# Kernel tuning notes

Hardware: AMD Instinct MI355X
Metric: run time of the kernel (lower is better)

## Reference

```python
import jax, jax.numpy as jnp
import numpy as np

N = 50000      # nodes
E = 300000     # edges per hop
H = 64         # hidden_channels
P = 3          # hops
DIRS = 3
L = 2          # num_layers
G = 50         # graphs in batch
FUS_IN = H * (2 + 2 * DIRS)  # 512
SLOPE = 0.01   # torch leaky_relu default negative slope


def setup_inputs():
    key = jax.random.key(0)
    ks = jax.random.split(key, 32)
    def nrm(k, shape, s=0.1):
        return jax.random.normal(k, shape, jnp.float32) * s
    return {
        "x": jax.random.normal(ks[0], (N, H), jnp.float32),
        "pe": jax.random.normal(ks[1], (N, DIRS), jnp.float32),
        "batch": jnp.sort(jax.random.randint(ks[2], (N,), 0, G, jnp.int32)),
        "u_edge_index": jax.random.randint(ks[3], (P, 2, E), 0, N, jnp.int32),
        "u_edge_weight": jax.random.uniform(ks[4], (P, E), jnp.float32),
        "f_edge_index": jax.random.randint(ks[5], (P, 2, E), 0, N, jnp.int32),
        "f_edge_weight": jax.random.uniform(ks[6], (P, E), jnp.float32),
        "emb_W": nrm(ks[7], (H, H)), "emb_b": nrm(ks[8], (H,)),
        "S_lin_W": nrm(ks[9], (L, H, H)), "S_lin_b": nrm(ks[10], (L, H)),
        "S_d": nrm(ks[11], (L, P, H), 1.0), "S_hb": nrm(ks[12], (L, P, H)),
        "S_fW": nrm(ks[13], (L, P, FUS_IN, H), 0.04), "S_fb": nrm(ks[14], (L, P, H)),
        "F_lin_W": nrm(ks[15], (L, H, H)), "F_lin_b": nrm(ks[16], (L, H)),
        "F_d": nrm(ks[17], (L, P, H), 1.0), "F_hb": nrm(ks[18], (L, P, H)),
        "F_fW": nrm(ks[19], (L, P, FUS_IN, H), 0.04), "F_fb": nrm(ks[20], (L, P, H)),
        "nS_w": 1.0 + nrm(ks[21], (L, H)), "nS_b": nrm(ks[22], (L, H)),
        "nS_m": 1.0 + nrm(ks[23], (L, H)),
        "nF_w": 1.0 + nrm(ks[24], (L, H)), "nF_b": nrm(ks[25], (L, H)),
        "nF_m": 1.0 + nrm(ks[26], (L, H)),
        "gate_W": nrm(ks[27], (2 * H, H)), "gate_b": nrm(ks[28], (H,)),
    }


def _opdmp(x, pe, ei, ew, lin_W, lin_b, d, hop_bias, fus_W, fus_b):
    """One OPDMPConv: multi-hop gather / scatter_add with directional weights."""
    x_t = x @ lin_W + lin_b              # [N, H]
    d_w = jax.nn.softmax(d, axis=0)      # [P, H]
    out = jnp.zeros_like(x_t)
    u = pe[:, :DIRS]
    for p in range(P):
        row, col, w = ei[p, 0], ei[p, 1], ew[p]
        # precompute() runs under torch.no_grad() -> stop_gradient
        deg = jax.ops.segment_sum(jax.lax.stop_gradient(w), row, num_segments=N)
        deg_inv = jnp.where(deg == 0.0, 0.0, 1.0 / deg)                  # [N]
        diff = jax.lax.stop_gradient(u[col] - u[row])                    # [E, DIRS]
        W2 = jnp.concatenate([jax.nn.relu(diff), jax.nn.relu(-diff)], axis=1)  # [E, 2*DIRS]
        xc = x_t[col]                                                    # [E, H] gather
        out_avg = jax.ops.segment_sum(xc * w[:, None], row, num_segments=N) * deg_inv[:, None]
        msg_dir = (xc[:, :, None] * W2[:, None, :]).reshape(E, H * 2 * DIRS)
        out_dir = jax.ops.segment_sum(msg_dir, row, num_segments=N) * deg_inv[:, None]
        h_cat = jnp.concatenate([x_t, out_avg, out_dir], axis=-1)        # [N, FUS_IN]
        h_p = jax.nn.leaky_relu(h_cat @ fus_W[p] + fus_b[p], SLOPE)
        out = out + h_p * d_w[p] + hop_bias[p]
    return out


def _graph_norm(x, batch, w, b, ms):
    cnt = jnp.maximum(jax.ops.segment_sum(jnp.ones((N,), x.dtype), batch, num_segments=G), 1.0)
    mean = jax.ops.segment_sum(x, batch, num_segments=G) / cnt[:, None]
    out = x - mean[batch] * ms
    var = jax.ops.segment_sum(out * out, batch, num_segments=G) / cnt[:, None]
    return out / jnp.sqrt(var[batch] + 1e-5) * w + b


def _forward(x, pe, u_edge_weight, f_edge_weight, emb_W, emb_b,
             S_lin_W, S_lin_b, S_d, S_hb, S_fW, S_fb,
             F_lin_W, F_lin_b, F_d, F_hb, F_fW, F_fb,
             nS_w, nS_b, nS_m, nF_w, nF_b, nF_m,
             gate_W, gate_b, batch, u_edge_index, f_edge_index):
    x = x @ emb_W + emb_b
    for i in range(L):
        prev = x
        h = _opdmp(x, pe, u_edge_index, u_edge_weight,
                   S_lin_W[i], S_lin_b[i], S_d[i], S_hb[i], S_fW[i], S_fb[i])
        h = jax.nn.leaky_relu(_graph_norm(h, batch, nS_w[i], nS_b[i], nS_m[i]), SLOPE)
        fx = _opdmp(h, pe, f_edge_index, f_edge_weight,
                    F_lin_W[i], F_lin_b[i], F_d[i], F_hb[i], F_fW[i], F_fb[i])
        fx = jax.nn.leaky_relu(_graph_norm(fx, batch, nF_w[i], nF_b[i], nF_m[i]), SLOPE)
        gate = jax.nn.sigmoid(jnp.concatenate([h, fx], axis=-1) @ gate_W + gate_b)
        x = gate * h + (1.0 - gate) * fx + prev   # dropout = identity in eval mode
    cnt = jnp.maximum(jax.ops.segment_sum(jnp.ones((N,), x.dtype), batch, num_segments=G), 1.0)
    return jax.ops.segment_sum(x, batch, num_segments=G) / cnt[:, None]  # global_mean_pool


def reference(x, pe, batch, u_edge_index, u_edge_weight, f_edge_index, f_edge_weight,
              emb_W, emb_b, S_lin_W, S_lin_b, S_d, S_hb, S_fW, S_fb,
              F_lin_W, F_lin_b, F_d, F_hb, F_fW, F_fb,
              nS_w, nS_b, nS_m, nF_w, nF_b, nF_m, gate_W, gate_b):
    return _forward(x, pe, u_edge_weight, f_edge_weight, emb_W, emb_b,
                    S_lin_W, S_lin_b, S_d, S_hb, S_fW, S_fb,
                    F_lin_W, F_lin_b, F_d, F_hb, F_fW, F_fb,
                    nS_w, nS_b, nS_m, nF_w, nF_b, nF_m,
                    gate_W, gate_b, batch, u_edge_index, f_edge_index)
```

## Files before the change

### kernel.cpp

```cpp
#include <hip/hip_runtime.h>
#include <cstdint>
#include <cstddef>

#define NN 50000
#define EE 300000
#define HH 64
#define PP 3
#define GG 50
#define LL 2
#define CAP 32
#define SLOPE 0.01f

typedef __attribute__((ext_vector_type(8))) short bf16x8;
typedef __attribute__((ext_vector_type(4))) float f32x4;

__device__ __forceinline__ float lrelu(float x){ return x >= 0.f ? x : SLOPE*x; }

__device__ __forceinline__ unsigned short f2bf(float x){
    uint32_t u = __float_as_uint(x);
    uint32_t r = (u + 0x7FFFu + ((u >> 16) & 1u)) >> 16;
    return (unsigned short)r;
}

__global__ void k_bounds(const int* __restrict__ batch, int* __restrict__ gstart){
    int g = threadIdx.x;
    if (g > GG) return;
    int lo = 0, hi = NN;
    while (lo < hi){ int mid = (lo + hi) >> 1; if (batch[mid] < g) lo = mid + 1; else hi = mid; }
    gstart[g] = lo;
}

__global__ void k_pe4(const float* __restrict__ pe, float4* __restrict__ pe4){
    int n = blockIdx.x * blockDim.x + threadIdx.x;
    if (n >= NN) return;
    pe4[n] = make_float4(pe[n * 3 + 0], pe[n * 3 + 1], pe[n * 3 + 2], 0.f);
}

__global__ void k_fill2(const int* __restrict__ uei, const float* __restrict__ uew,
                        const int* __restrict__ fei, const float* __restrict__ few,
                        int* __restrict__ cnt, int2* __restrict__ bucket){
    int t = blockIdx.x * blockDim.x + threadIdx.x;
    if (t >= 2 * PP * EE) return;
    int which = t / EE;
    int e = t - which * EE;
    const int* ei; const float* ew; int p;
    if (which < PP){ ei = uei; ew = uew; p = which; }
    else           { ei = fei; ew = few; p = which - PP; }
    int row = ei[(size_t)(p * 2 + 0) * EE + e];
    int col = ei[(size_t)(p * 2 + 1) * EE + e];
    float w = ew[(size_t)p * EE + e];
    int slot = atomicAdd(cnt + (size_t)which * NN + row, 1);
    if (slot < CAP)
        bucket[((size_t)which * NN + row) * CAP + slot] = make_int2(col, __float_as_int(w));
}

__global__ void k_wpermb(const float* __restrict__ S_fW, const float* __restrict__ F_fW,
                         unsigned short* __restrict__ Wpb){
    int gid = blockIdx.x * blockDim.x + threadIdx.x;
    int j = gid & 7;
    int lane = (gid >> 3) & 63;
    int w = (gid >> 9) & 3;
    int kb = (gid >> 11) & 15;
    int t = gid >> 15;
    int q = kb * 32 + (lane >> 4) * 8 + j;
    int col = w * 16 + (lane & 15);
    int conv = t / 6, layer = (t % 6) / 3, p = t % 3;
    const float* src = (conv ? F_fW : S_fW) + ((size_t)layer * PP + p) * 512 * HH;
    int kref;
    if (q < 128) kref = q;
    else { int r = q - 128; kref = 128 + (r & 63) * 6 + (r >> 6); }
    Wpb[gid] = f2bf(src[(size_t)kref * HH + col]);
}

__global__ __launch_bounds__(256) void k_lin64(const float* __restrict__ X,
                       const float* __restrict__ W, const float* __restrict__ b,
                       float* __restrict__ out){
    __shared__ float xs[32][HH];
    int nb = blockIdx.x * 32;
    int t = threadIdx.x;
    #pragma unroll
    for (int i = 0; i < 2; ++i){
        int idx = t + 256 * i;
        int r = idx >> 4, c4 = idx & 15;
        int n = nb + r;
        float4 v = make_float4(0.f, 0.f, 0.f, 0.f);
        if (n < NN) v = *reinterpret_cast<const float4*>(X + (size_t)n * HH + c4 * 4);
        *reinterpret_cast<float4*>(&xs[r][c4 * 4]) = v;
    }
    __syncthreads();
    int lane = t & 63, wave = t >> 6, nw = wave * 8;
    float acc[8];
    float bb = b[lane];
    #pragma unroll
    for (int i = 0; i < 8; ++i) acc[i] = bb;
    #pragma unroll 2
    for (int k = 0; k < HH; ++k){
        float wv = W[(size_t)k * HH + lane];
        #pragma unroll
        for (int i = 0; i < 8; ++i) acc[i] += xs[nw + i][k] * wv;
    }
    #pragma unroll
    for (int i = 0; i < 8; ++i){
        int n = nb + nw + i;
        if (n < NN) out[(size_t)n * HH + lane] = acc[i];
    }
}

__global__ __launch_bounds__(256) void k_hop3(const float* __restrict__ xt,
        const int* __restrict__ cnt, const int2* __restrict__ bucket,
        const float4* __restrict__ pe4, const unsigned short* __restrict__ Wpb3,
        const float* __restrict__ fb3, const float* __restrict__ dmat,
        const float* __restrict__ hb3, float* __restrict__ outb){
    __shared__ unsigned short u[16][512];
    int nb = blockIdx.x * 16;
    int t = threadIdx.x;
    int lane = t & 63, wave = t >> 6, nw = wave * 4;
    {
        int r = t >> 4, c4 = t & 15;
        float4 v = *reinterpret_cast<const float4*>(xt + (size_t)(nb + r) * HH + c4 * 4);
        ushort4 s;
        s.x = f2bf(v.x); s.y = f2bf(v.y); s.z = f2bf(v.z); s.w = f2bf(v.w);
        int q = (c4 * 4) ^ ((r & 7) << 3);
        *reinterpret_cast<ushort4*>(&u[r][q]) = s;
    }
    int c = wave * 16 + (lane & 15);
    float d0 = dmat[c], d1 = dmat[64 + c], d2 = dmat[128 + c];
    float mx = fmaxf(d0, fmaxf(d1, d2));
    float e0 = expf(d0 - mx), e1 = expf(d1 - mx), e2 = expf(d2 - mx);
    float esum = e0 + e1 + e2;
    float dw0 = e0 / esum, dw1 = e1 / esum, dw2 = e2 / esum;
    float accOut[4];
    float hbs = hb3[c] + hb3[64 + c] + hb3[128 + c];
    #pragma unroll
    for (int r = 0; r < 4; ++r) accOut[r] = hbs;

    for (int p = 0; p < 3; ++p){
        __syncthreads();
        const int*  cntp = cnt + (size_t)p * NN;
        const int2* bp   = bucket + (size_t)p * NN * CAP;
        #pragma unroll
        for (int i = 0; i < 4; ++i){
            int n = nb + nw + i;
            float accA = 0.f, sumw = 0.f;
            float a0 = 0.f, a1 = 0.f, a2 = 0.f, a3 = 0.f, a4 = 0.f, a5 = 0.f;
            int len = cntp[n]; if (len > CAP) len = CAP;
            const int2* b = bp + (size_t)n * CAP;
            float4 pr = pe4[n];
            int  cols[8];
            float ws[8];
            #pragma unroll
            for (int s = 0; s < 8; ++s){
                int2 m = b[s];
                bool ok = (s < len);
                cols[s] = ok ? m.x : n;
                ws[s]   = ok ? __int_as_float(m.y) : 0.f;
            }
            float4 pcs[8];
            float  xvs[8];
            #pragma unroll
            for (int s = 0; s < 8; ++s){
                pcs[s] = pe4[cols[s]];
                xvs[s] = xt[(size_t)cols[s] * HH + lane];
            }
            #pragma unroll
            for (int s = 0; s < 8; ++s){
                float w = ws[s], xv = xvs[s];
                float dd0 = pcs[s].x - pr.x;
                float dd1 = pcs[s].y - pr.y;
                float dd2 = pcs[s].z - pr.z;
                sumw += w;  accA += w * xv;
                a0 += fmaxf(dd0, 0.f) * xv;  a3 += fmaxf(-dd0, 0.f) * xv;
                a1 += fmaxf(dd1, 0.f) * xv;  a4 += fmaxf(-dd1, 0.f) * xv;
                a2 += fmaxf(dd2, 0.f) * xv;  a5 += fmaxf(-dd2, 0.f) * xv;
            }
            for (int s = 8; s < len; ++s){
                int2 m = b[s];
                int col = m.x;
                float w = __int_as_float(m.y);
                float4 pc = pe4[col];
                float xv = xt[(size_t)col * HH + lane];
                float dd0 = pc.x - pr.x;
                float dd1 = pc.y - pr.y;
                float dd2 = pc.z - pr.z;
                sumw += w;  accA += w * xv;
                a0 += fmaxf(dd0, 0.f) * xv;  a3 += fmaxf(-dd0, 0.f) * xv;
                a1 += fmaxf(dd1, 0.f) * xv;  a4 += fmaxf(-dd1, 0.f) * xv;
                a2 += fmaxf(dd2, 0.f) * xv;  a5 += fmaxf(-dd2, 0.f) * xv;
            }
            float di = (sumw == 0.f) ? 0.f : 1.f / sumw;
            int il = nw + i;
            int sw = (il & 7) << 3;
            u[il][(64 + lane) ^ sw]           = f2bf(accA * di);
            u[il][(128 + 0 * 64 + lane) ^ sw] = f2bf(a0 * di);
            u[il][(128 + 1 * 64 + lane) ^ sw] = f2bf(a1 * di);
            u[il][(128 + 2 * 64 + lane) ^ sw] = f2bf(a2 * di);
            u[il][(128 + 3 * 64 + lane) ^ sw] = f2bf(a3 * di);
            u[il][(128 + 4 * 64 + lane) ^ sw] = f2bf(a4 * di);
            u[il][(128 + 5 * 64 + lane) ^ sw] = f2bf(a5 * di);
        }
        __syncthreads();
        const unsigned short* wb = Wpb3 + (size_t)p * 32768;
        f32x4 acc = {0.f, 0.f, 0.f, 0.f};
        int arow = lane & 15;
        int asw = (arow & 7) << 3;
        #pragma unroll
        for (int kb = 0; kb < 16; ++kb){
            int qa = (kb * 32 + (lane >> 4) * 8) ^ asw;
            bf16x8 a = *reinterpret_cast<const bf16x8*>(&u[arow][qa]);
            bf16x8 b = *reinterpret_cast<const bf16x8*>(&wb[(((size_t)kb * 4 + wave) * 64 + lane) * 8]);
            acc = __builtin_amdgcn_mfma_f32_16x16x32_bf16(a, b, acc, 0, 0, 0);
        }
        float fbv = fb3[p * 64 + c];
        float dw = (p == 0) ? dw0 : ((p == 1) ? dw1 : dw2);
        #pragma unroll
        for (int r = 0; r < 4; ++r)
            accOut[r] += lrelu(acc[r] + fbv) * dw;
    }
    #pragma unroll
    for (int r = 0; r < 4; ++r){
        int row = (lane >> 4) * 4 + r;
        outb[(size_t)(nb + row) * HH + c] = accOut[r];
    }
}

__global__ void k_stats(const float* __restrict__ X, const int* __restrict__ gstart,
                        float* __restrict__ sums, float* __restrict__ sumsq){
    int g = blockIdx.x;
    int tid = threadIdx.x;
    int o = tid & 63, sub = tid >> 6;
    int ns = gstart[g], ne = gstart[g + 1];
    float s = 0.f, q = 0.f;
    for (int n = ns + sub; n < ne; n += 16){
        float v = X[(size_t)n * 64 + o];
        s += v; q += v * v;
    }
    __shared__ float ls[16][64];
    __shared__ float lq[16][64];
    ls[sub][o] = s; lq[sub][o] = q;
    __syncthreads();
    if (sub == 0){
        #pragma unroll
        for (int k = 1; k < 16; ++k){ s += ls[k][o]; q += lq[k][o]; }
        sums[g * 64 + o] = s;
        sumsq[g * 64 + o] = q;
    }
}

__global__ void k_gnorm(float* __restrict__ X, const int* __restrict__ batch,
                        const int* __restrict__ gstart,
                        const float* __restrict__ sums, const float* __restrict__ sumsq,
                        const float* __restrict__ w, const float* __restrict__ b,
                        const float* __restrict__ ms){
    int gid = blockIdx.x * blockDim.x + threadIdx.x;
    if (gid >= NN * HH) return;
    int n = gid >> 6, o = gid & 63;
    int g = batch[n];
    float cnt = fmaxf((float)(gstart[g + 1] - gstart[g]), 1.f);
    float mean = sums[g * 64 + o] / cnt;
    float ex2 = sumsq[g * 64 + o] / cnt;
    float m = ms[o];
    float var = ex2 - mean * mean * m * (2.f - m);
    float v = (X[gid] - mean * m) * (1.f / sqrtf(var + 1e-5f)) * w[o] + b[o];
    X[gid] = lrelu(v);
}

__global__ __launch_bounds__(256) void k_gate2(const float* __restrict__ h,
                       const float* __restrict__ fx, const float* __restrict__ gW,
                       const float* __restrict__ gb, float* __restrict__ X){
    __shared__ float hs[32][HH];
    __shared__ float fs[32][HH];
    int nb = blockIdx.x * 32;
    int t = threadIdx.x;
    #pragma unroll
    for (int i = 0; i < 2; ++i){
        int idx = t + 256 * i;
        int r = idx >> 4, c4 = idx & 15;
        int n = nb + r;
        float4 vh = make_float4(0.f, 0.f, 0.f, 0.f);
        float4 vf = make_float4(0.f, 0.f, 0.f, 0.f);
        if (n < NN){
            vh = *reinterpret_cast<const float4*>(h  + (size_t)n * HH + c4 * 4);
            vf = *reinterpret_cast<const float4*>(fx + (size_t)n * HH + c4 * 4);
        }
        *reinterpret_cast<float4*>(&hs[r][c4 * 4]) = vh;
        *reinterpret_cast<float4*>(&fs[r][c4 * 4]) = vf;
    }
    __syncthreads();
    int lane = t & 63, wave = t >> 6, nw = wave * 8;
    float acc[8];
    float bb = gb[lane];
    #pragma unroll
    for (int i = 0; i < 8; ++i) acc[i] = bb;
    #pragma unroll 2
    for (int k = 0; k < HH; ++k){
        float w1 = gW[(size_t)k * HH + lane];
        float w2 = gW[(size_t)(64 + k) * HH + lane];
        #pragma unroll
        for (int i = 0; i < 8; ++i) acc[i] += hs[nw + i][k] * w1 + fs[nw + i][k] * w2;
    }
    #pragma unroll
    for (int i = 0; i < 8; ++i){
        int n = nb + nw + i;
        if (n < NN){
            float gt = 1.f / (1.f + expf(-acc[i]));
            float hv = hs[nw + i][lane];
            float fv = fs[nw + i][lane];
            size_t idx = (size_t)n * HH + lane;
            X[idx] = gt * hv + (1.f - gt) * fv + X[idx];
        }
    }
}

__global__ void k_finalout(const float* __restrict__ sums, const int* __restrict__ gstart,
                           float* __restrict__ out){
    int gid = blockIdx.x * blockDim.x + threadIdx.x;
    if (gid >= GG * HH) return;
    int g = gid >> 6;
    float cnt = fmaxf((float)(gstart[g + 1] - gstart[g]), 1.f);
    out[gid] = sums[gid] / cnt;
}

extern "C" void kernel_launch(void* const* d_in, const int* in_sizes, int n_in,
                              void* d_out, int out_size, void* d_ws, size_t ws_size,
                              hipStream_t stream) {
    const float* x_in   = (const float*)d_in[0];
    const float* pe     = (const float*)d_in[1];
    const int*   batch  = (const int*)d_in[2];
    const int*   uei    = (const int*)d_in[3];
    const float* uew    = (const float*)d_in[4];
    const int*   fei    = (const int*)d_in[5];
    const float* few    = (const float*)d_in[6];
    const float* emb_W  = (const float*)d_in[7];
    const float* emb_b  = (const float*)d_in[8];
    const float* S_lin_W= (const float*)d_in[9];
    const float* S_lin_b= (const float*)d_in[10];
    const float* S_d    = (const float*)d_in[11];
    const float* S_hb   = (const float*)d_in[12];
    const float* S_fW   = (const float*)d_in[13];
    const float* S_fb   = (const float*)d_in[14];
    const float* F_lin_W= (const float*)d_in[15];
    const float* F_lin_b= (const float*)d_in[16];
    const float* F_d    = (const float*)d_in[17];
    const float* F_hb   = (const float*)d_in[18];
    const float* F_fW   = (const float*)d_in[19];
    const float* F_fb   = (const float*)d_in[20];
    const float* nS_w   = (const float*)d_in[21];
    const float* nS_b   = (const float*)d_in[22];
    const float* nS_m   = (const float*)d_in[23];
    const float* nF_w   = (const float*)d_in[24];
    const float* nF_b   = (const float*)d_in[25];
    const float* nF_m   = (const float*)d_in[26];
    const float* gate_W = (const float*)d_in[27];
    const float* gate_b = (const float*)d_in[28];
    float* out = (float*)d_out;

    size_t off = 0;
    auto alloc = [&](size_t bytes)->void*{
        void* p = (char*)d_ws + off;
        off += (bytes + 255) & ~(size_t)255;
        return p;
    };
    float*  xbuf   = (float*)alloc((size_t)NN * HH * 4);
    float*  hbuf   = (float*)alloc((size_t)NN * HH * 4);
    float*  fxbuf  = (float*)alloc((size_t)NN * HH * 4);
    float*  xt     = (float*)alloc((size_t)NN * HH * 4);
    unsigned short* Wpb12 = (unsigned short*)alloc((size_t)12 * 32768 * 2);
    float4* pe4    = (float4*)alloc((size_t)NN * 16);
    int*    cnt    = (int*)  alloc((size_t)6 * NN * 4);
    int2*   bucket = (int2*) alloc((size_t)6 * NN * CAP * 8);
    int*    gstart = (int*)  alloc((GG + 1) * 4);
    float*  sums   = (float*)alloc(GG * HH * 4);
    float*  sumsq  = (float*)alloc(GG * HH * 4);

    const int BLK = 256;
    const int gridNH = (NN * HH) / BLK;
    const int gridN32 = (NN + 31) / 32;
    const int gridHop = NN / 16;
    const int gridEdges = (2 * PP * EE + BLK - 1) / BLK;
    const int gridWb = (12 * 32768) / BLK;

    k_bounds<<<1, 64, 0, stream>>>(batch, gstart);
    k_pe4<<<(NN + BLK - 1) / BLK, BLK, 0, stream>>>(pe, pe4);
    hipMemsetAsync(cnt, 0, (size_t)6 * NN * 4, stream);
    k_fill2<<<gridEdges, BLK, 0, stream>>>(uei, uew, fei, few, cnt, bucket);
    k_wpermb<<<gridWb, BLK, 0, stream>>>(S_fW, F_fW, Wpb12);
    k_lin64<<<gridN32, BLK, 0, stream>>>(x_in, emb_W, emb_b, xbuf);

    auto gnorm = [&](float* X, const float* w, const float* b, const float* ms){
        k_stats<<<GG, 1024, 0, stream>>>(X, gstart, sums, sumsq);
        k_gnorm<<<gridNH, BLK, 0, stream>>>(X, batch, gstart, sums, sumsq, w, b, ms);
    };

    for (int i = 0; i < LL; ++i){
        k_lin64<<<gridN32, BLK, 0, stream>>>(xbuf, S_lin_W + (size_t)i * HH * HH,
                                             S_lin_b + (size_t)i * HH, xt);
        k_hop3<<<gridHop, BLK, 0, stream>>>(xt, cnt, bucket, pe4,
                Wpb12 + (size_t)(0 * 6 + i * 3) * 32768,
                S_fb + (size_t)i * PP * HH, S_d + (size_t)i * PP * HH,
                S_hb + (size_t)i * PP * HH, hbuf);
        gnorm(hbuf, nS_w + (size_t)i * HH, nS_b + (size_t)i * HH, nS_m + (size_t)i * HH);
        k_lin64<<<gridN32, BLK, 0, stream>>>(hbuf, F_lin_W + (size_t)i * HH * HH,
                                             F_lin_b + (size_t)i * HH, xt);
        k_hop3<<<gridHop, BLK, 0, stream>>>(xt, cnt + (size_t)PP * NN,
                bucket + (size_t)PP * NN * CAP, pe4,
                Wpb12 + (size_t)(1 * 6 + i * 3) * 32768,
                F_fb + (size_t)i * PP * HH, F_d + (size_t)i * PP * HH,
                F_hb + (size_t)i * PP * HH, fxbuf);
        gnorm(fxbuf, nF_w + (size_t)i * HH, nF_b + (size_t)i * HH, nF_m + (size_t)i * HH);
        k_gate2<<<gridN32, BLK, 0, stream>>>(hbuf, fxbuf, gate_W, gate_b, xbuf);
    }

    k_stats<<<GG, 1024, 0, stream>>>(xbuf, gstart, sums, sumsq);
    k_finalout<<<(GG * HH + BLK - 1) / BLK, BLK, 0, stream>>>(sums, gstart, out);
}
```

Baseline: 1.220 ms.

## Store transformed features in bf16, batch second gather chunk, split graph stats

```diff
diff --git a/kernel.cpp b/kernel.cpp
--- a/kernel.cpp
+++ b/kernel.cpp
@@ -20,6 +20,9 @@
     uint32_t u = __float_as_uint(x);
     uint32_t r = (u + 0x7FFFu + ((u >> 16) & 1u)) >> 16;
     return (unsigned short)r;
+}
+__device__ __forceinline__ float bf2f(unsigned short s){
+    return __uint_as_float((uint32_t)s << 16);
 }
 
 __global__ void k_bounds(const int* __restrict__ batch, int* __restrict__ gstart){
@@ -106,7 +109,41 @@
     }
 }
 
-__global__ __launch_bounds__(256) void k_hop3(const float* __restrict__ xt,
+__global__ __launch_bounds__(256) void k_lin64b(const float* __restrict__ X,
+                       const float* __restrict__ W, const float* __restrict__ b,
+                       unsigned short* __restrict__ out){
+    __shared__ float xs[32][HH];
+    int nb = blockIdx.x * 32;
+    int t = threadIdx.x;
+    #pragma unroll
+    for (int i = 0; i < 2; ++i){
+        int idx = t + 256 * i;
+        int r = idx >> 4, c4 = idx & 15;
+        int n = nb + r;
+        float4 v = make_float4(0.f, 0.f, 0.f, 0.f);
+        if (n < NN) v = *reinterpret_cast<const float4*>(X + (size_t)n * HH + c4 * 4);
+        *reinterpret_cast<float4*>(&xs[r][c4 * 4]) = v;
+    }
+    __syncthreads();
+    int lane = t & 63, wave = t >> 6, nw = wave * 8;
+    float acc[8];
+    float bb = b[lane];
+    #pragma unroll
+    for (int i = 0; i < 8; ++i) acc[i] = bb;
+    #pragma unroll 2
+    for (int k = 0; k < HH; ++k){
+        float wv = W[(size_t)k * HH + lane];
+        #pragma unroll
+        for (int i = 0; i < 8; ++i) acc[i] += xs[nw + i][k] * wv;
+    }
+    #pragma unroll
+    for (int i = 0; i < 8; ++i){
+        int n = nb + nw + i;
+        if (n < NN) out[(size_t)n * HH + lane] = f2bf(acc[i]);
+    }
+}
+
+__global__ __launch_bounds__(256) void k_hop3(const unsigned short* __restrict__ xtb,
         const int* __restrict__ cnt, const int2* __restrict__ bucket,
         const float4* __restrict__ pe4, const unsigned short* __restrict__ Wpb3,
         const float* __restrict__ fb3, const float* __restrict__ dmat,
@@ -117,9 +154,7 @@
     int lane = t & 63, wave = t >> 6, nw = wave * 4;
     {
         int r = t >> 4, c4 = t & 15;
-        float4 v = *reinterpret_cast<const float4*>(xt + (size_t)(nb + r) * HH + c4 * 4);
-        ushort4 s;
-        s.x = f2bf(v.x); s.y = f2bf(v.y); s.z = f2bf(v.z); s.w = f2bf(v.w);
+        ushort4 s = *reinterpret_cast<const ushort4*>(xtb + (size_t)(nb + r) * HH + c4 * 4);
         int q = (c4 * 4) ^ ((r & 7) << 3);
         *reinterpret_cast<ushort4*>(&u[r][q]) = s;
     }
@@ -146,39 +181,66 @@
             int len = cntp[n]; if (len > CAP) len = CAP;
             const int2* b = bp + (size_t)n * CAP;
             float4 pr = pe4[n];
-            int  cols[8];
-            float ws[8];
-            #pragma unroll
-            for (int s = 0; s < 8; ++s){
-                int2 m = b[s];
-                bool ok = (s < len);
-                cols[s] = ok ? m.x : n;
-                ws[s]   = ok ? __int_as_float(m.y) : 0.f;
+            {
+                int  cols[8]; float ws[8];
+                #pragma unroll
+                for (int s = 0; s < 8; ++s){
+                    int2 m = b[s];
+                    bool ok = (s < len);
+                    cols[s] = ok ? m.x : n;
+                    ws[s]   = ok ? __int_as_float(m.y) : 0.f;
+                }
+                float4 pcs[8]; float xvs[8];
+                #pragma unroll
+                for (int s = 0; s < 8; ++s){
+                    pcs[s] = pe4[cols[s]];
+                    xvs[s] = bf2f(xtb[(size_t)cols[s] * HH + lane]);
+                }
+                #pragma unroll
+                for (int s = 0; s < 8; ++s){
+                    float w = ws[s], xv = xvs[s];
+                    float dd0 = pcs[s].x - pr.x;
+                    float dd1 = pcs[s].y - pr.y;
+                    float dd2 = pcs[s].z - pr.z;
+                    sumw += w;  accA += w * xv;
+                    a0 += fmaxf(dd0, 0.f) * xv;  a3 += fmaxf(-dd0, 0.f) * xv;
+                    a1 += fmaxf(dd1, 0.f) * xv;  a4 += fmaxf(-dd1, 0.f) * xv;
+                    a2 += fmaxf(dd2, 0.f) * xv;  a5 += fmaxf(-dd2, 0.f) * xv;
+                }
             }
-            float4 pcs[8];
-            float  xvs[8];
-            #pragma unroll
-            for (int s = 0; s < 8; ++s){
-                pcs[s] = pe4[cols[s]];
-                xvs[s] = xt[(size_t)cols[s] * HH + lane];
+            if (len > 8){
+                int  cols[8]; float ws[8];
+                #pragma unroll
+                for (int s = 0; s < 8; ++s){
+                    int2 m = b[8 + s];
+                    bool ok = (8 + s < len);
+                    cols[s] = ok ? m.x : n;
+                    ws[s]   = ok ? __int_as_float(m.y) : 0.f;
+                }
+                float4 pcs[8]; float xvs[8];
+                #pragma unroll
+                for (int s = 0; s < 8; ++s){
+                    pcs[s] = pe4[cols[s]];
+                    xvs[s] = bf2f(xtb[(size_t)cols[s] * HH + lane]);
+                }
+                #pragma unroll
+                for (int s = 0; s < 8; ++s){
+                    float w = ws[s], xv = xvs[s];
+                    float dd0 = pcs[s].x - pr.x;
+                    float dd1 = pcs[s].y - pr.y;
+                    float dd2 = pcs[s].z - pr.z;
+                    sumw += w;  accA += w * xv;
+                    a0 += fmaxf(dd0, 0.f) * xv;  a3 += fmaxf(-dd0, 0.f) * xv;
+                    a1 += fmaxf(dd1, 0.f) * xv;  a4 += fmaxf(-dd1, 0.f) * xv;
+                    a2 += fmaxf(dd2, 0.f) * xv;  a5 += fmaxf(-dd2, 0.f) * xv;
+                }
             }
-            #pragma unroll
-            for (int s = 0; s < 8; ++s){
-                float w = ws[s], xv = xvs[s];
-                float dd0 = pcs[s].x - pr.x;
-                float dd1 = pcs[s].y - pr.y;
-                float dd2 = pcs[s].z - pr.z;
-                sumw += w;  accA += w * xv;
-                a0 += fmaxf(dd0, 0.f) * xv;  a3 += fmaxf(-dd0, 0.f) * xv;
-                a1 += fmaxf(dd1, 0.f) * xv;  a4 += fmaxf(-dd1, 0.f) * xv;
-                a2 += fmaxf(dd2, 0.f) * xv;  a5 += fmaxf(-dd2, 0.f) * xv;
-            }
-            for (int s = 8; s < len; ++s){
+            for (int s = 16; s < len; ++s){
                 int2 m = b[s];
                 int col = m.x;
                 float w = __int_as_float(m.y);
                 float4 pc = pe4[col];
-                float xv = xt[(size_t)col * HH + lane];
+                float xv = bf2f(xtb[(size_t)col * HH + lane]);
                 float dd0 = pc.x - pr.x;
                 float dd1 = pc.y - pr.y;
                 float dd2 = pc.z - pr.z;
@@ -223,32 +285,31 @@
     }
 }
 
-__global__ void k_stats(const float* __restrict__ X, const int* __restrict__ gstart,
-                        float* __restrict__ sums, float* __restrict__ sumsq){
-    int g = blockIdx.x;
-    int tid = threadIdx.x;
-    int o = tid & 63, sub = tid >> 6;
+__global__ void k_stats4(const float* __restrict__ X, const int* __restrict__ gstart,
+                         float* __restrict__ sums4, float* __restrict__ sumsq4){
+    int g = blockIdx.x, chunk = blockIdx.y;
+    int o = threadIdx.x & 63, sub = threadIdx.x >> 6;
     int ns = gstart[g], ne = gstart[g + 1];
     float s = 0.f, q = 0.f;
-    for (int n = ns + sub; n < ne; n += 16){
+    for (int n = ns + chunk * 4 + sub; n < ne; n += 16){
         float v = X[(size_t)n * 64 + o];
         s += v; q += v * v;
     }
-    __shared__ float ls[16][64];
-    __shared__ float lq[16][64];
+    __shared__ float ls[4][64];
+    __shared__ float lq[4][64];
     ls[sub][o] = s; lq[sub][o] = q;
     __syncthreads();
     if (sub == 0){
         #pragma unroll
-        for (int k = 1; k < 16; ++k){ s += ls[k][o]; q += lq[k][o]; }
-        sums[g * 64 + o] = s;
-        sumsq[g * 64 + o] = q;
+        for (int k = 1; k < 4; ++k){ s += ls[k][o]; q += lq[k][o]; }
+        sums4 [(size_t)(chunk * GG + g) * 64 + o] = s;
+        sumsq4[(size_t)(chunk * GG + g) * 64 + o] = q;
     }
 }
 
 __global__ void k_gnorm(float* __restrict__ X, const int* __restrict__ batch,
                         const int* __restrict__ gstart,
-                        const float* __restrict__ sums, const float* __restrict__ sumsq,
+                        const float* __restrict__ sums4, const float* __restrict__ sumsq4,
                         const float* __restrict__ w, const float* __restrict__ b,
                         const float* __restrict__ ms){
     int gid = blockIdx.x * blockDim.x + threadIdx.x;
@@ -256,8 +317,14 @@
     int n = gid >> 6, o = gid & 63;
     int g = batch[n];
     float cnt = fmaxf((float)(gstart[g + 1] - gstart[g]), 1.f);
-    float mean = sums[g * 64 + o] / cnt;
-    float ex2 = sumsq[g * 64 + o] / cnt;
+    float sm = 0.f, sq = 0.f;
+    #pragma unroll
+    for (int cC = 0; cC < 4; ++cC){
+        sm += sums4 [(size_t)(cC * GG + g) * 64 + o];
+        sq += sumsq4[(size_t)(cC * GG + g) * 64 + o];
+    }
+    float mean = sm / cnt;
+    float ex2 = sq / cnt;
     float m = ms[o];
     float var = ex2 - mean * mean * m * (2.f - m);
     float v = (X[gid] - mean * m) * (1.f / sqrtf(var + 1e-5f)) * w[o] + b[o];
@@ -311,13 +378,16 @@
     }
 }
 
-__global__ void k_finalout(const float* __restrict__ sums, const int* __restrict__ gstart,
+__global__ void k_finalout(const float* __restrict__ sums4, const int* __restrict__ gstart,
                            float* __restrict__ out){
     int gid = blockIdx.x * blockDim.x + threadIdx.x;
     if (gid >= GG * HH) return;
-    int g = gid >> 6;
+    int g = gid >> 6, o = gid & 63;
     float cnt = fmaxf((float)(gstart[g + 1] - gstart[g]), 1.f);
-    out[gid] = sums[gid] / cnt;
+    float sm = 0.f;
+    #pragma unroll
+    for (int cC = 0; cC < 4; ++cC) sm += sums4[(size_t)(cC * GG + g) * 64 + o];
+    out[gid] = sm / cnt;
 }
 
 extern "C" void kernel_launch(void* const* d_in, const int* in_sizes, int n_in,
@@ -363,14 +433,14 @@
     float*  xbuf   = (float*)alloc((size_t)NN * HH * 4);
     float*  hbuf   = (float*)alloc((size_t)NN * HH * 4);
     float*  fxbuf  = (float*)alloc((size_t)NN * HH * 4);
-    float*  xt     = (float*)alloc((size_t)NN * HH * 4);
+    unsigned short* xtb = (unsigned short*)alloc((size_t)NN * HH * 2);
     unsigned short* Wpb12 = (unsigned short*)alloc((size_t)12 * 32768 * 2);
     float4* pe4    = (float4*)alloc((size_t)NN * 16);
     int*    cnt    = (int*)  alloc((size_t)6 * NN * 4);
     int2*   bucket = (int2*) alloc((size_t)6 * NN * CAP * 8);
     int*    gstart = (int*)  alloc((GG + 1) * 4);
-    float*  sums   = (float*)alloc(GG * HH * 4);
-    float*  sumsq  = (float*)alloc(GG * HH * 4);
+    float*  sums4  = (float*)alloc((size_t)4 * GG * HH * 4);
+    float*  sumsq4 = (float*)alloc((size_t)4 * GG * HH * 4);
 
     const int BLK = 256;
     const int gridNH = (NN * HH) / BLK;
@@ -387,21 +457,21 @@
     k_lin64<<<gridN32, BLK, 0, stream>>>(x_in, emb_W, emb_b, xbuf);
 
     auto gnorm = [&](float* X, const float* w, const float* b, const float* ms){
-        k_stats<<<GG, 1024, 0, stream>>>(X, gstart, sums, sumsq);
-        k_gnorm<<<gridNH, BLK, 0, stream>>>(X, batch, gstart, sums, sumsq, w, b, ms);
+        k_stats4<<<dim3(GG, 4), BLK, 0, stream>>>(X, gstart, sums4, sumsq4);
+        k_gnorm<<<gridNH, BLK, 0, stream>>>(X, batch, gstart, sums4, sumsq4, w, b, ms);
     };
 
     for (int i = 0; i < LL; ++i){
-        k_lin64<<<gridN32, BLK, 0, stream>>>(xbuf, S_lin_W + (size_t)i * HH * HH,
-                                             S_lin_b + (size_t)i * HH, xt);
-        k_hop3<<<gridHop, BLK, 0, stream>>>(xt, cnt, bucket, pe4,
+        k_lin64b<<<gridN32, BLK, 0, stream>>>(xbuf, S_lin_W + (size_t)i * HH * HH,
+                                              S_lin_b + (size_t)i * HH, xtb);
+        k_hop3<<<gridHop, BLK, 0, stream>>>(xtb, cnt, bucket, pe4,
                 Wpb12 + (size_t)(0 * 6 + i * 3) * 32768,
                 S_fb + (size_t)i * PP * HH, S_d + (size_t)i * PP * HH,
                 S_hb + (size_t)i * PP * HH, hbuf);
         gnorm(hbuf, nS_w + (size_t)i * HH, nS_b + (size_t)i * HH, nS_m + (size_t)i * HH);
-        k_lin64<<<gridN32, BLK, 0, stream>>>(hbuf, F_lin_W + (size_t)i * HH * HH,
-                                             F_lin_b + (size_t)i * HH, xt);
-        k_hop3<<<gridHop, BLK, 0, stream>>>(xt, cnt + (size_t)PP * NN,
+        k_lin64b<<<gridN32, BLK, 0, stream>>>(hbuf, F_lin_W + (size_t)i * HH * HH,
+                                              F_lin_b + (size_t)i * HH, xtb);
+        k_hop3<<<gridHop, BLK, 0, stream>>>(xtb, cnt + (size_t)PP * NN,
                 bucket + (size_t)PP * NN * CAP, pe4,
                 Wpb12 + (size_t)(1 * 6 + i * 3) * 32768,
                 F_fb + (size_t)i * PP * HH, F_d + (size_t)i * PP * HH,
@@ -410,6 +480,6 @@
         k_gate2<<<gridN32, BLK, 0, stream>>>(hbuf, fxbuf, gate_W, gate_b, xbuf);
     }
 
-    k_stats<<<GG, 1024, 0, stream>>>(xbuf, gstart, sums, sumsq);
-    k_finalout<<<(GG * HH + BLK - 1) / BLK, BLK, 0, stream>>>(sums, gstart, out);
-}
+    k_stats4<<<dim3(GG, 4), BLK, 0, stream>>>(xbuf, gstart, sums4, sumsq4);
+    k_finalout<<<(GG * HH + BLK - 1) / BLK, BLK, 0, stream>>>(sums4, gstart, out);
+}
```

Measured after the change: 1.032 ms. 15.4% less time.
